# Kernel optimization log

Measured on AMD Instinct MI355X. Metric: run time of the kernel, lower is better.

Reference implementation:

```python
import jax, jax.numpy as jnp
import numpy as np
import math

B, T, C = 4, 2048, 1024
N_HEAD = 16
HEAD_DIM = C // N_HEAD


def setup_inputs() -> dict:
    key = jax.random.key(0)
    k1, k2, k3, k4, k5 = jax.random.split(key, 5)
    s = 1.0 / math.sqrt(C)
    return {
        "x": jax.random.normal(k1, (B, T, C), dtype=jnp.float32),
        "W_attn": jax.random.normal(k2, (3 * C, C), dtype=jnp.float32) * s,
        "b_attn": jax.random.normal(k3, (3 * C,), dtype=jnp.float32) * 0.02,
        "W_proj": jax.random.normal(k4, (C, C), dtype=jnp.float32) * s,
        "b_proj": jax.random.normal(k5, (C,), dtype=jnp.float32) * 0.02,
    }


def reference(x, W_attn, b_attn, W_proj, b_proj):
    Bx, Tx, Cx = x.shape
    # QKV projection (torch Linear: x @ W.T + b), split into q,k,v
    qkv = jnp.einsum("btc,dc->btd", x, W_attn) + b_attn  # [B,T,3C]
    q, k, v = jnp.split(qkv, 3, axis=-1)
    # [B,T,C] -> [B,H,T,hd]
    def to_heads(t):
        return t.reshape(Bx, Tx, N_HEAD, HEAD_DIM).transpose(0, 2, 1, 3)
    q, k, v = to_heads(q), to_heads(k), to_heads(v)
    scale = 1.0 / math.sqrt(HEAD_DIM)
    att = jnp.einsum("bhqd,bhkd->bhqk", q, k) * scale  # [B,H,T,T]
    causal = jnp.tril(jnp.ones((Tx, Tx), dtype=bool))
    att = jnp.where(causal, att, -jnp.inf)
    att = jax.nn.softmax(att, axis=-1)
    y = jnp.einsum("bhqk,bhkd->bhqd", att, v)  # [B,H,T,hd]
    y = y.transpose(0, 2, 1, 3).reshape(Bx, Tx, Cx)
    y = jnp.einsum("btc,dc->btd", y, W_proj) + b_proj
    return y
```

## Files before the change

### kernel.cpp

```cpp
#include <hip/hip_runtime.h>
#include <hip/hip_bf16.h>
#include <stdint.h>

typedef unsigned short u16;
typedef __attribute__((ext_vector_type(8))) short bf16x8;
typedef __attribute__((ext_vector_type(4))) short s16x4;
typedef __attribute__((ext_vector_type(4))) float f32x4;

#define B_SZ 4
#define T_SZ 2048
#define C_SZ 1024
#define NH   16
#define HD   64
#define LOG2E 1.44269504088896340736f

__device__ __forceinline__ u16 f2bf(float f) {
  unsigned int u = __float_as_uint(f);
  u += 0x7fffu + ((u >> 16) & 1u);
  return (u16)(u >> 16);
}
__device__ __forceinline__ u16 f2bf_hu(float f) {
  return (u16)((__float_as_uint(f) + 0x8000u) >> 16);
}
__device__ __forceinline__ void gload_lds16(const u16* g, u16* l) {
  __builtin_amdgcn_global_load_lds((const __attribute__((address_space(1))) void*)g,
                                   (__attribute__((address_space(3))) void*)l, 16, 0, 0);
}

__global__ void cast_f32_bf16(const float* __restrict__ in, u16* __restrict__ out, int n8) {
  int i = blockIdx.x * blockDim.x + threadIdx.x;
  if (i < n8) {
    const float4* p = (const float4*)in + (size_t)i * 2;
    float4 a = p[0], b = p[1];
    bf16x8 o;
    o[0] = (short)f2bf(a.x); o[1] = (short)f2bf(a.y);
    o[2] = (short)f2bf(a.z); o[3] = (short)f2bf(a.w);
    o[4] = (short)f2bf(b.x); o[5] = (short)f2bf(b.y);
    o[6] = (short)f2bf(b.z); o[7] = (short)f2bf(b.w);
    ((bf16x8*)out)[i] = o;
  }
}

template <int MODE>
__launch_bounds__(256, 3)
__global__ void gemm_bt(const u16* __restrict__ A, const u16* __restrict__ Bw,
                        const float* __restrict__ bias,
                        void* __restrict__ O0, void* __restrict__ O1, void* __restrict__ O2,
                        int M, int N, int K) {
  __shared__ __align__(16) u16 As[128 * 32];
  __shared__ __align__(16) u16 Bs[128 * 32];
  const int tid = threadIdx.x;
  const int lane = tid & 63;
  const int w = tid >> 6;
  const int wr = w >> 1, wc = w & 1;
  const int quad = lane >> 4, l16 = lane & 15;
  const int m0 = blockIdx.y * 128;
  const int n0 = blockIdx.x * 128;

  const int srow = lane >> 2;
  const int scol = (lane & 3) * 8;
  const u16* gA = A + (size_t)(m0 + w * 32 + srow) * K + scol;
  const u16* gB = Bw + (size_t)(n0 + w * 32 + srow) * K + scol;
  u16* lA0 = &As[(w * 32) * 32];
  u16* lA1 = &As[(w * 32 + 16) * 32];
  u16* lB0 = &Bs[(w * 32) * 32];
  u16* lB1 = &Bs[(w * 32 + 16) * 32];
  const size_t rstep = (size_t)16 * K;

  f32x4 acc[4][4];
#pragma unroll
  for (int i = 0; i < 4; i++)
#pragma unroll
    for (int j = 0; j < 4; j++) acc[i][j] = (f32x4){0.f, 0.f, 0.f, 0.f};

  for (int k0 = 0; k0 < K; k0 += 32) {
    __syncthreads();
    gload_lds16(gA + k0, lA0);
    gload_lds16(gA + rstep + k0, lA1);
    gload_lds16(gB + k0, lB0);
    gload_lds16(gB + rstep + k0, lB1);
    __syncthreads();
    bf16x8 af[4], bfr[4];
#pragma unroll
    for (int mt = 0; mt < 4; mt++)
      af[mt] = *(const bf16x8*)&As[(wr * 64 + mt * 16 + l16) * 32 + quad * 8];
#pragma unroll
    for (int nt = 0; nt < 4; nt++)
      bfr[nt] = *(const bf16x8*)&Bs[(wc * 64 + nt * 16 + l16) * 32 + quad * 8];
#pragma unroll
    for (int mt = 0; mt < 4; mt++)
#pragma unroll
      for (int nt = 0; nt < 4; nt++)
        acc[mt][nt] = __builtin_amdgcn_mfma_f32_16x16x32_bf16(af[mt], bfr[nt], acc[mt][nt], 0, 0, 0);
  }

  float bv[4];
#pragma unroll
  for (int nt = 0; nt < 4; nt++) bv[nt] = bias[n0 + wc * 64 + nt * 16 + l16];

  if (MODE == 0) {
    float* Cout = (float*)O0;
#pragma unroll
    for (int mt = 0; mt < 4; mt++) {
      const int row = m0 + wr * 64 + mt * 16 + quad * 4;
#pragma unroll
      for (int nt = 0; nt < 4; nt++) {
        const int col = n0 + wc * 64 + nt * 16 + l16;
#pragma unroll
        for (int r = 0; r < 4; r++)
          Cout[(size_t)(row + r) * N + col] = acc[mt][nt][r] + bv[nt];
      }
    }
  } else {
    const int nsec = (n0 + wc * 64) >> 10;
    const int hh = ((n0 + wc * 64) >> 6) & 15;
    if (nsec < 2) {
      u16* dst = (u16*)(nsec == 0 ? O0 : O1);
#pragma unroll
      for (int mt = 0; mt < 4; mt++) {
        const int row = m0 + wr * 64 + mt * 16 + quad * 4;
        const int bb = row >> 11;
        const int t = row & 2047;
#pragma unroll
        for (int nt = 0; nt < 4; nt++) {
          const int dh = nt * 16 + l16;
          const size_t a = (((size_t)bb * NH + hh) * T_SZ + t) * HD + dh;
#pragma unroll
          for (int r = 0; r < 4; r++)
            dst[a + (size_t)r * HD] = f2bf(acc[mt][nt][r] + bv[nt]);
        }
      }
    } else {
      u16* vth = (u16*)O2;
#pragma unroll
      for (int mt = 0; mt < 4; mt++) {
        const int row = m0 + wr * 64 + mt * 16 + quad * 4;
        const int bb = row >> 11;
        const int t = row & 2047;
#pragma unroll
        for (int nt = 0; nt < 4; nt++) {
          const int dh = nt * 16 + l16;
          s16x4 pk;
#pragma unroll
          for (int r = 0; r < 4; r++) pk[r] = (short)f2bf(acc[mt][nt][r] + bv[nt]);
          *(s16x4*)&vth[(((size_t)bb * NH + hh) * HD + dh) * T_SZ + t] = pk;
        }
      }
    }
  }
}

__device__ __forceinline__ void attn_step(
    int kb, int kbn, int w, int quad, int l16, int qt128, int sw0, int sw1,
    const u16* gK0, const u16* gK1, const u16* gV0, const u16* gV1,
    u16* KsF, u16* VsF, u16* PsW,
    const bf16x8 (&qf)[2][2], f32x4 (&o)[2][4], float (&l_i)[2][4]) {
  __syncthreads();

  if (kb + 1 < kbn) {
    const int nb = (kb + 1) & 1;
    const size_t ko = (size_t)(kb + 1) * 64 * HD;
    const int vo = (kb + 1) * 64;
    gload_lds16(gK0 + ko, KsF + nb * 4096 + (2 * w) * 512);
    gload_lds16(gK1 + ko, KsF + nb * 4096 + (2 * w + 1) * 512);
    gload_lds16(gV0 + vo, VsF + nb * 4096 + (2 * w) * 512);
    gload_lds16(gV1 + vo, VsF + nb * 4096 + (2 * w + 1) * 512);
  }

  const u16* Kb = KsF + (kb & 1) * 4096;
  const u16* Vb = VsF + (kb & 1) * 4096;
  const int kt0 = kb * 64;
  const float SC = 0.125f * LOG2E;

#pragma unroll
  for (int m = 0; m < 2; m++) {
    const int mrow = qt128 + w * 32 + m * 16;
    const int qr = mrow + quad * 4;
    const bool diag = (kt0 + 64 > mrow);

    f32x4 s[4];
    __builtin_amdgcn_s_setprio(1);
#pragma unroll
    for (int nt = 0; nt < 4; nt++) {
      bf16x8 kf0 = *(const bf16x8*)&Kb[(nt * 16 + l16) * 64 + sw0];
      bf16x8 kf1 = *(const bf16x8*)&Kb[(nt * 16 + l16) * 64 + sw1];
      f32x4 t0 = (f32x4){0.f, 0.f, 0.f, 0.f};
      t0 = __builtin_amdgcn_mfma_f32_16x16x32_bf16(qf[m][0], kf0, t0, 0, 0, 0);
      t0 = __builtin_amdgcn_mfma_f32_16x16x32_bf16(qf[m][1], kf1, t0, 0, 0, 0);
      s[nt] = t0;
    }
    __builtin_amdgcn_s_setprio(0);

    if (diag) {
#pragma unroll
      for (int nt = 0; nt < 4; nt++) {
        const int dk = kt0 + nt * 16 + l16 - qr;
#pragma unroll
        for (int r = 0; r < 4; r++) {
          float v = (dk > r) ? -10000.f : s[nt][r] * SC;
          s[nt][r] = exp2f(v);
        }
      }
    } else {
#pragma unroll
      for (int nt = 0; nt < 4; nt++)
#pragma unroll
        for (int r = 0; r < 4; r++)
          s[nt][r] = exp2f(s[nt][r] * SC);
    }
#pragma unroll
    for (int r = 0; r < 4; r++)
      l_i[m][r] += (s[0][r] + s[1][r]) + (s[2][r] + s[3][r]);

#pragma unroll
    for (int nt = 0; nt < 4; nt++)
#pragma unroll
      for (int r = 0; r < 4; r++)
        PsW[(quad * 4 + r) * 72 + nt * 16 + l16] = f2bf_hu(s[nt][r]);
    bf16x8 p0 = *(const bf16x8*)&PsW[l16 * 72 + quad * 8];
    bf16x8 p1 = *(const bf16x8*)&PsW[l16 * 72 + 32 + quad * 8];
    __builtin_amdgcn_s_setprio(1);
#pragma unroll
    for (int nt = 0; nt < 4; nt++) {
      bf16x8 v0 = *(const bf16x8*)&Vb[(nt * 16 + l16) * 64 + sw0];
      bf16x8 v1 = *(const bf16x8*)&Vb[(nt * 16 + l16) * 64 + sw1];
      o[m][nt] = __builtin_amdgcn_mfma_f32_16x16x32_bf16(p0, v0, o[m][nt], 0, 0, 0);
      o[m][nt] = __builtin_amdgcn_mfma_f32_16x16x32_bf16(p1, v1, o[m][nt], 0, 0, 0);
    }
    __builtin_amdgcn_s_setprio(0);
  }
}

__launch_bounds__(256, 3)
__global__ void attn_fused(const u16* __restrict__ qh, const u16* __restrict__ kh,
                           const u16* __restrict__ vth, u16* __restrict__ out) {
  __shared__ __align__(16) u16 Ks[2][64 * 64];
  __shared__ __align__(16) u16 Vs[2][64 * 64];
  __shared__ __align__(16) u16 Ps[4][16 * 72];
  const int qt = 15 - blockIdx.z;
  const int h = blockIdx.x, b = blockIdx.y;
  const int tid = threadIdx.x;
  const int lane = tid & 63, w = tid >> 6;
  const int quad = lane >> 4, l16 = lane & 15;
  const size_t bh = (size_t)b * NH + h;
  const u16* Kbase = kh + bh * T_SZ * HD;
  const u16* Vbase = vth + bh * HD * T_SZ;
  const int qt128 = qt * 128;

  const int dr = lane >> 3;
  const int dc = (lane & 7) ^ dr;
  const u16* gK0 = Kbase + (size_t)(2 * w * 8 + dr) * HD + dc * 8;
  const u16* gK1 = Kbase + (size_t)((2 * w + 1) * 8 + dr) * HD + dc * 8;
  const u16* gV0 = Vbase + (size_t)(2 * w * 8 + dr) * T_SZ + dc * 8;
  const u16* gV1 = Vbase + (size_t)((2 * w + 1) * 8 + dr) * T_SZ + dc * 8;
  u16* KsF = &Ks[0][0];
  u16* VsF = &Vs[0][0];
  u16* PsW = &Ps[w][0];

  bf16x8 qf[2][2];
#pragma unroll
  for (int m = 0; m < 2; m++) {
    const int t = qt128 + w * 32 + m * 16 + l16;
    const u16* qrow = qh + (bh * T_SZ + t) * HD;
    qf[m][0] = *(const bf16x8*)(qrow + quad * 8);
    qf[m][1] = *(const bf16x8*)(qrow + 32 + quad * 8);
  }

  f32x4 o[2][4];
  float l_i[2][4];
#pragma unroll
  for (int m = 0; m < 2; m++)
#pragma unroll
    for (int i = 0; i < 4; i++) {
      o[m][i] = (f32x4){0.f, 0.f, 0.f, 0.f};
      l_i[m][i] = 0.f;
    }

  const int kbn = 2 * qt + 2;
  const int sw0 = (quad ^ (l16 & 7)) * 8;
  const int sw1 = ((4 + quad) ^ (l16 & 7)) * 8;

  gload_lds16(gK0, KsF + (2 * w) * 512);
  gload_lds16(gK1, KsF + (2 * w + 1) * 512);
  gload_lds16(gV0, VsF + (2 * w) * 512);
  gload_lds16(gV1, VsF + (2 * w + 1) * 512);

  for (int kb = 0; kb < kbn; kb++)
    attn_step(kb, kbn, w, quad, l16, qt128, sw0, sw1,
              gK0, gK1, gV0, gV1, KsF, VsF, PsW, qf, o, l_i);

#pragma unroll
  for (int m = 0; m < 2; m++)
#pragma unroll
    for (int r = 0; r < 4; r++) {
      float v = l_i[m][r];
      v += __shfl_xor(v, 1);
      v += __shfl_xor(v, 2);
      v += __shfl_xor(v, 4);
      v += __shfl_xor(v, 8);
      const float inv = 1.f / v;
      const int t = qt128 + w * 32 + m * 16 + quad * 4 + r;
      const size_t orow = ((size_t)b * T_SZ + t) * C_SZ + (size_t)h * HD;
#pragma unroll
      for (int nt = 0; nt < 4; nt++)
        out[orow + nt * 16 + l16] = f2bf(o[m][nt][r] * inv);
    }
}

extern "C" void kernel_launch(void* const* d_in, const int* in_sizes, int n_in,
                              void* d_out, int out_size, void* d_ws, size_t ws_size,
                              hipStream_t stream) {
  (void)in_sizes; (void)n_in; (void)out_size; (void)ws_size;
  const float* x      = (const float*)d_in[0];
  const float* W_attn = (const float*)d_in[1];
  const float* b_attn = (const float*)d_in[2];
  const float* W_proj = (const float*)d_in[3];
  const float* b_proj = (const float*)d_in[4];
  float* out = (float*)d_out;

  char* ws = (char*)d_ws;
  u16* xb  = (u16*)ws;  ws += (size_t)8192 * 1024 * 2;
  u16* Wab = (u16*)ws;  ws += (size_t)3072 * 1024 * 2;
  u16* Wpb = (u16*)ws;  ws += (size_t)1024 * 1024 * 2;
  u16* qhb = (u16*)ws;  ws += (size_t)8192 * 1024 * 2;
  u16* khb = (u16*)ws;  ws += (size_t)8192 * 1024 * 2;
  u16* vtb = (u16*)ws;  ws += (size_t)8192 * 1024 * 2;
  u16* aob = (u16*)ws;

  dim3 blk(256);
  cast_f32_bf16<<<(8192 * 1024 / 8 + 255) / 256, blk, 0, stream>>>(x, xb, 8192 * 1024 / 8);
  cast_f32_bf16<<<(3072 * 1024 / 8 + 255) / 256, blk, 0, stream>>>(W_attn, Wab, 3072 * 1024 / 8);
  cast_f32_bf16<<<(1024 * 1024 / 8 + 255) / 256, blk, 0, stream>>>(W_proj, Wpb, 1024 * 1024 / 8);

  gemm_bt<1><<<dim3(3072 / 128, 8192 / 128), blk, 0, stream>>>(
      xb, Wab, b_attn, qhb, khb, vtb, 8192, 3072, 1024);
  attn_fused<<<dim3(NH, B_SZ, 16), blk, 0, stream>>>(qhb, khb, vtb, aob);
  gemm_bt<0><<<dim3(1024 / 128, 8192 / 128), blk, 0, stream>>>(
      aob, Wpb, b_proj, out, nullptr, nullptr, 8192, 1024, 1024);
}
```

Measured before the change: 267.7 us.

## Replace GEMM with 256x256 tile, 8-wave, double-buffered swizzled-LDS pipelined kernel

```diff
diff --git a/kernel.cpp b/kernel.cpp
--- a/kernel.cpp
+++ b/kernel.cpp
@@ -42,83 +42,149 @@
 }
 
 template <int MODE>
-__launch_bounds__(256, 3)
-__global__ void gemm_bt(const u16* __restrict__ A, const u16* __restrict__ Bw,
-                        const float* __restrict__ bias,
-                        void* __restrict__ O0, void* __restrict__ O1, void* __restrict__ O2,
-                        int M, int N, int K) {
-  __shared__ __align__(16) u16 As[128 * 32];
-  __shared__ __align__(16) u16 Bs[128 * 32];
+__launch_bounds__(512, 2)
+__global__ void gemm8(const u16* __restrict__ A, const u16* __restrict__ Bw,
+                      const float* __restrict__ bias,
+                      void* __restrict__ O0, void* __restrict__ O1, void* __restrict__ O2,
+                      int M, int N, int K) {
+  extern __shared__ u16 lds[];
+  u16* As = lds;
+  u16* Bs = lds + 32768;
   const int tid = threadIdx.x;
-  const int lane = tid & 63;
-  const int w = tid >> 6;
-  const int wr = w >> 1, wc = w & 1;
+  const int lane = tid & 63, w = tid >> 6;
+  const int wm = w >> 2, wn = w & 3;
   const int quad = lane >> 4, l16 = lane & 15;
-  const int m0 = blockIdx.y * 128;
-  const int n0 = blockIdx.x * 128;
-
-  const int srow = lane >> 2;
-  const int scol = (lane & 3) * 8;
-  const u16* gA = A + (size_t)(m0 + w * 32 + srow) * K + scol;
-  const u16* gB = Bw + (size_t)(n0 + w * 32 + srow) * K + scol;
-  u16* lA0 = &As[(w * 32) * 32];
-  u16* lA1 = &As[(w * 32 + 16) * 32];
-  u16* lB0 = &Bs[(w * 32) * 32];
-  u16* lB1 = &Bs[(w * 32 + 16) * 32];
-  const size_t rstep = (size_t)16 * K;
-
-  f32x4 acc[4][4];
-#pragma unroll
-  for (int i = 0; i < 4; i++)
+
+  const int gx = gridDim.x;
+  const int nwg = gx * gridDim.y;
+  const int wg0 = blockIdx.y * gx + blockIdx.x;
+  const int swz = (wg0 & 7) * (nwg >> 3) + (wg0 >> 3);
+  const int n0 = (swz % gx) * 256;
+  const int m0 = (swz / gx) * 256;
+
+  const int dr8 = lane >> 3;
+  const int dc8 = (lane & 7) ^ dr8;
+  const u16* gAL = A + (size_t)(m0 + w * 8 + dr8) * K + dc8 * 8;
+  const u16* gBL = Bw + (size_t)(n0 + w * 8 + dr8) * K + dc8 * 8;
+  u16* dA = As + w * 512;
+  u16* dB = Bs + w * 512;
+
+  const int NT = K >> 6;
+
+  auto stageA = [&](int tile) {
+    u16* d = dA + (tile & 1) * 16384;
+    const u16* g = gAL + (size_t)tile * 64;
+#pragma unroll
+    for (int h = 0; h < 2; ++h)
+#pragma unroll
+      for (int i = 0; i < 2; ++i)
+        gload_lds16(g + (size_t)(h * 128 + i * 64) * K, d + h * 8192 + i * 4096);
+  };
+  auto stageB = [&](int tile, int h) {
+    u16* d = dB + (tile & 1) * 16384 + h * 8192;
+    const u16* g = gBL + (size_t)tile * 64 + (size_t)h * 128 * K;
+#pragma unroll
+    for (int i = 0; i < 2; ++i)
+      gload_lds16(g + (size_t)i * 64 * K, d + i * 4096);
+  };
+
+  f32x4 acc[8][4];
+#pragma unroll
+  for (int i = 0; i < 8; i++)
 #pragma unroll
     for (int j = 0; j < 4; j++) acc[i][j] = (f32x4){0.f, 0.f, 0.f, 0.f};
 
-  for (int k0 = 0; k0 < K; k0 += 32) {
-    __syncthreads();
-    gload_lds16(gA + k0, lA0);
-    gload_lds16(gA + rstep + k0, lA1);
-    gload_lds16(gB + k0, lB0);
-    gload_lds16(gB + rstep + k0, lB1);
-    __syncthreads();
-    bf16x8 af[4], bfr[4];
-#pragma unroll
-    for (int mt = 0; mt < 4; mt++)
-      af[mt] = *(const bf16x8*)&As[(wr * 64 + mt * 16 + l16) * 32 + quad * 8];
-#pragma unroll
-    for (int nt = 0; nt < 4; nt++)
-      bfr[nt] = *(const bf16x8*)&Bs[(wc * 64 + nt * 16 + l16) * 32 + quad * 8];
-#pragma unroll
-    for (int mt = 0; mt < 4; mt++)
-#pragma unroll
-      for (int nt = 0; nt < 4; nt++)
-        acc[mt][nt] = __builtin_amdgcn_mfma_f32_16x16x32_bf16(af[mt], bfr[nt], acc[mt][nt], 0, 0, 0);
+  stageA(0);
+  stageB(0, 0); stageB(0, 1);
+  stageB(1, 0); stageB(1, 1);
+  asm volatile("s_waitcnt vmcnt(4)" ::: "memory");
+  __builtin_amdgcn_s_barrier();
+
+  const u16* AbaseR = As + wm * 8192;
+  const u16* BbaseR = Bs + (wn >> 1) * 8192 + (wn & 1) * 64 * 64;
+  const int sK0 = ((quad) ^ (l16 & 7)) * 8;
+  const int sK1 = ((4 + quad) ^ (l16 & 7)) * 8;
+
+  const int NIT = NT >> 1;
+  for (int j = 0; j < NIT; ++j) {
+#pragma unroll
+    for (int tt = 0; tt < 2; ++tt) {
+      const int tile = 2 * j + tt;
+      const int bufo = (tile & 1) * 16384;
+      const u16* Ab = AbaseR + bufo;
+      const u16* Bb = BbaseR + bufo;
+      bf16x8 bfr[4][2];
+#pragma unroll
+      for (int mp = 0; mp < 4; ++mp) {
+        bf16x8 af[2][2];
+#pragma unroll
+        for (int a2 = 0; a2 < 2; ++a2) {
+          const int ro = ((mp * 2 + a2) * 16 + l16) * 64;
+          af[a2][0] = *(const bf16x8*)&Ab[ro + sK0];
+          af[a2][1] = *(const bf16x8*)&Ab[ro + sK1];
+        }
+        if (mp == 0) {
+#pragma unroll
+          for (int nt = 0; nt < 4; ++nt) {
+            const int ro = (nt * 16 + l16) * 64;
+            bfr[nt][0] = *(const bf16x8*)&Bb[ro + sK0];
+            bfr[nt][1] = *(const bf16x8*)&Bb[ro + sK1];
+          }
+        }
+        if (mp == 0) { if (tile + 1 < NT) stageA(tile + 1); }
+        else if (mp == 1) { if (tile + 2 < NT) stageB(tile + 2, 0); }
+        else if (mp == 2) { if (tile + 2 < NT) stageB(tile + 2, 1); }
+        if (mp == 0) asm volatile("s_waitcnt lgkmcnt(8)");
+        asm volatile("" ::: "memory");
+        __builtin_amdgcn_s_barrier();
+        asm volatile("s_waitcnt lgkmcnt(0)" ::: "memory");
+        __builtin_amdgcn_sched_barrier(0);
+        __builtin_amdgcn_s_setprio(1);
+#pragma unroll
+        for (int a2 = 0; a2 < 2; ++a2)
+#pragma unroll
+          for (int nt = 0; nt < 4; ++nt) {
+            f32x4 c = acc[mp * 2 + a2][nt];
+            c = __builtin_amdgcn_mfma_f32_16x16x32_bf16(af[a2][0], bfr[nt][0], c, 0, 0, 0);
+            c = __builtin_amdgcn_mfma_f32_16x16x32_bf16(af[a2][1], bfr[nt][1], c, 0, 0, 0);
+            acc[mp * 2 + a2][nt] = c;
+          }
+        __builtin_amdgcn_s_setprio(0);
+        if (mp == 3) {
+          if (tile + 2 >= NT) asm volatile("s_waitcnt vmcnt(0)" ::: "memory");
+          else                asm volatile("s_waitcnt vmcnt(4)" ::: "memory");
+        }
+        asm volatile("" ::: "memory");
+        __builtin_amdgcn_s_barrier();
+      }
+    }
   }
 
   float bv[4];
 #pragma unroll
-  for (int nt = 0; nt < 4; nt++) bv[nt] = bias[n0 + wc * 64 + nt * 16 + l16];
+  for (int nt = 0; nt < 4; nt++) bv[nt] = bias[n0 + wn * 64 + nt * 16 + l16];
 
   if (MODE == 0) {
     float* Cout = (float*)O0;
 #pragma unroll
-    for (int mt = 0; mt < 4; mt++) {
-      const int row = m0 + wr * 64 + mt * 16 + quad * 4;
+    for (int mt = 0; mt < 8; mt++) {
+      const int row = m0 + wm * 128 + mt * 16 + quad * 4;
 #pragma unroll
       for (int nt = 0; nt < 4; nt++) {
-        const int col = n0 + wc * 64 + nt * 16 + l16;
+        const int col = n0 + wn * 64 + nt * 16 + l16;
 #pragma unroll
         for (int r = 0; r < 4; r++)
           Cout[(size_t)(row + r) * N + col] = acc[mt][nt][r] + bv[nt];
       }
     }
   } else {
-    const int nsec = (n0 + wc * 64) >> 10;
-    const int hh = ((n0 + wc * 64) >> 6) & 15;
+    const int nsec = (n0 + wn * 64) >> 10;
+    const int hh = ((n0 + wn * 64) >> 6) & 15;
     if (nsec < 2) {
       u16* dst = (u16*)(nsec == 0 ? O0 : O1);
 #pragma unroll
-      for (int mt = 0; mt < 4; mt++) {
-        const int row = m0 + wr * 64 + mt * 16 + quad * 4;
+      for (int mt = 0; mt < 8; mt++) {
+        const int row = m0 + wm * 128 + mt * 16 + quad * 4;
         const int bb = row >> 11;
         const int t = row & 2047;
 #pragma unroll
@@ -133,8 +199,8 @@
     } else {
       u16* vth = (u16*)O2;
 #pragma unroll
-      for (int mt = 0; mt < 4; mt++) {
-        const int row = m0 + wr * 64 + mt * 16 + quad * 4;
+      for (int mt = 0; mt < 8; mt++) {
+        const int row = m0 + wm * 128 + mt * 16 + quad * 4;
         const int bb = row >> 11;
         const int t = row & 2047;
 #pragma unroll
@@ -332,9 +398,9 @@
   cast_f32_bf16<<<(3072 * 1024 / 8 + 255) / 256, blk, 0, stream>>>(W_attn, Wab, 3072 * 1024 / 8);
   cast_f32_bf16<<<(1024 * 1024 / 8 + 255) / 256, blk, 0, stream>>>(W_proj, Wpb, 1024 * 1024 / 8);
 
-  gemm_bt<1><<<dim3(3072 / 128, 8192 / 128), blk, 0, stream>>>(
+  gemm8<1><<<dim3(3072 / 256, 8192 / 256), dim3(512), 131072, stream>>>(
       xb, Wab, b_attn, qhb, khb, vtb, 8192, 3072, 1024);
   attn_fused<<<dim3(NH, B_SZ, 16), blk, 0, stream>>>(qhb, khb, vtb, aob);
-  gemm_bt<0><<<dim3(1024 / 128, 8192 / 128), blk, 0, stream>>>(
+  gemm8<0><<<dim3(1024 / 256, 8192 / 256), dim3(512), 131072, stream>>>(
       aob, Wpb, b_proj, out, nullptr, nullptr, 8192, 1024, 1024);
 }
```

Measured after the change: 266.3 us. Within noise of the previous version (-0.5%).
